# Optimization experiments

Measured on AMD Instinct MI355X. Metric: run time of the kernel, lower is better.

## Reference

```python
import jax, jax.numpy as jnp
import numpy as np
from math import ceil, sqrt

# Inner module: Linear(2048,4096)+ReLU, Linear(4096,4096)+ReLU, Linear(4096,2048)
D_IN, D_H, D_OUT = 2048, 4096, 2048
BATCH = 4096
# named_modules() order: each Linear yields weight then bias; ReLU skipped
SHAPES = [(D_H, D_IN), (D_H,), (D_H, D_H), (D_H,), (D_OUT, D_H), (D_OUT,)]
NUM_P = sum(int(np.prod(s)) for s in SHAPES)  # 33_566_720
SIZE_N = ceil(sqrt(NUM_P))                    # 5794
SIZE_M = ceil(1.0 * SIZE_N / 2)               # 2897 (compress = 1.0)


def setup_inputs() -> dict:
    key = jax.random.key(0)
    k1, k2, k3 = jax.random.split(key, 3)
    k = sqrt(12) / 2 * SIZE_M ** (-0.25)  # norm_V init bound
    V1 = jax.random.uniform(k1, (SIZE_N, SIZE_M), jnp.float32, -k, k)
    V2 = jax.random.uniform(k2, (SIZE_M, SIZE_N), jnp.float32, -k, k)
    x = jax.random.normal(k3, (BATCH, D_IN), jnp.float32)
    return {"x": x, "V1": V1, "V2": V2}


def _unpack(Vf):
    # scatter-copy: contiguous slices of flattened V -> weights/biases in traversal order
    params, i = [], 0
    for s in SHAPES:
        n = int(np.prod(s))
        params.append(Vf[i:i + n].reshape(s))
        i += n
    return params


def reference(x, V1, V2):
    # WandBtoV: low-rank reconstruction then per-element copy into weights (fused here)
    Vf = (V1 @ V2).reshape(-1)  # [SIZE_N*SIZE_N]; only first NUM_P elements used
    W1, b1, W2, b2, W3, b3 = _unpack(Vf)
    h = jax.nn.relu(x @ W1.T + b1)   # [B, D_H]
    h = jax.nn.relu(h @ W2.T + b2)   # [B, D_H]
    return h @ W3.T + b3             # [B, D_OUT]
```

## Files before the change

### kernel.cpp

```cpp
#include <hip/hip_runtime.h>
#include <stdint.h>

typedef __attribute__((ext_vector_type(8)))  __bf16 bf16x8;
typedef __attribute__((ext_vector_type(16))) float  f32x16;
typedef unsigned short u16;
typedef __attribute__((ext_vector_type(8))) unsigned short u16x8;

#define GLOBAL_AS __attribute__((address_space(1)))
#define LDS_AS    __attribute__((address_space(3)))

__device__ __forceinline__ void load_lds16(const void* g, void* l) {
    __builtin_amdgcn_global_load_lds((const GLOBAL_AS void*)g, (LDS_AS void*)l, 16, 0, 0);
}

__device__ __forceinline__ u16 f2bf(float f) {
    union { float f; uint32_t u; } v; v.f = f;
    uint32_t r = v.u + 0x7FFFu + ((v.u >> 16) & 1u);
    return (u16)(r >> 16);
}
__device__ __forceinline__ float b2f(u16 b) {
    union { uint32_t u; float f; } v; v.u = ((uint32_t)b) << 16;
    return v.f;
}

__global__ void k_conv_pad(const float* __restrict__ in, u16* __restrict__ out,
                           int rIn, int cIn, int cOut, int total8) {
    int idx = blockIdx.x * blockDim.x + threadIdx.x;
    if (idx >= total8) return;
    int c8n = cOut >> 3;
    int r  = idx / c8n;
    int c0 = (idx - r * c8n) << 3;
    u16x8 o;
#pragma unroll
    for (int j = 0; j < 8; ++j) {
        int c = c0 + j;
        o[j] = (r < rIn && c < cIn) ? f2bf(in[(size_t)r * cIn + c]) : (u16)0;
    }
    *(u16x8*)(out + (size_t)r * cOut + c0) = o;
}

__global__ void k_transpose_conv(const float* __restrict__ in, u16* __restrict__ out,
                                 int kIn, int nIn, int kOut) {
    __shared__ float tile[32][33];
    int k0 = blockIdx.x * 32, n0 = blockIdx.y * 32;
    int tx = threadIdx.x, ty = threadIdx.y;
#pragma unroll
    for (int i = 0; i < 4; ++i) {
        int k = k0 + ty + i * 8, n = n0 + tx;
        tile[ty + i * 8][tx] = (k < kIn && n < nIn) ? in[(size_t)k * nIn + n] : 0.f;
    }
    __syncthreads();
#pragma unroll
    for (int i = 0; i < 4; ++i) {
        int n = n0 + ty + i * 8, k = k0 + tx;
        out[(size_t)n * kOut + k] = f2bf(tile[tx][ty + i * 8]);
    }
}

template <int MODE>
__global__ __launch_bounds__(256, 4) void k_gemm_bt(
    const u16* __restrict__ A, const u16* __restrict__ B,
    const u16* __restrict__ bias, void* __restrict__ Cv,
    int K, int ldc, int mReal, int nReal) {
    (void)bias;
    __shared__ __align__(16) char lds[32768];
    char* As = lds;
    char* Bs = lds + 16384;

    const int tid  = threadIdx.x;
    const int w    = tid >> 6, lane = tid & 63;
    const int l31  = lane & 31, hi = lane >> 5;
    const int wm   = (w & 1) * 64, wn = (w >> 1) * 64;
    const int bm   = blockIdx.y * 128, bn = blockIdx.x * 128;

    const int srcRow = tid >> 3;
    const int srcCol = (tid & 7) ^ (srcRow & 7);
    const u16* aSrc = A + (size_t)(bm + srcRow) * K + (srcCol << 3);
    const u16* bSrc = B + (size_t)(bn + srcRow) * K + (srcCol << 3);
    char* aDst = As + ((tid & ~63) << 4);
    char* bDst = Bs + ((tid & ~63) << 4);

    const int aRow0 = (wm + l31) * 128;
    const int aRow1 = (wm + 32 + l31) * 128;
    const int bRow0 = (wn + l31) * 128;
    const int bRow1 = (wn + 32 + l31) * 128;

    f32x16 acc[2][2];
#pragma unroll
    for (int i = 0; i < 2; ++i)
#pragma unroll
        for (int j = 0; j < 2; ++j) acc[i][j] = (f32x16)(0.f);

    for (int k0 = 0; k0 < K; k0 += 64) {
#pragma unroll
        for (int t = 0; t < 4; ++t) {
            load_lds16(aSrc + (size_t)(t * 32) * K, aDst + t * 4096);
            load_lds16(bSrc + (size_t)(t * 32) * K, bDst + t * 4096);
        }
        aSrc += 64; bSrc += 64;
        __syncthreads();
#pragma unroll
        for (int ks = 0; ks < 4; ++ks) {
            const int swz = (((ks * 2 + hi) ^ (l31 & 7)) << 4);
            bf16x8 af[2], bfr[2];
            af[0]  = *(const bf16x8*)(As + aRow0 + swz);
            af[1]  = *(const bf16x8*)(As + aRow1 + swz);
            bfr[0] = *(const bf16x8*)(Bs + bRow0 + swz);
            bfr[1] = *(const bf16x8*)(Bs + bRow1 + swz);
#pragma unroll
            for (int mi = 0; mi < 2; ++mi)
#pragma unroll
                for (int ni = 0; ni < 2; ++ni)
                    acc[mi][ni] = __builtin_amdgcn_mfma_f32_32x32x16_bf16(
                        af[mi], bfr[ni], acc[mi][ni], 0, 0, 0);
        }
        __syncthreads();
    }

    float bv[2];
    if (MODE >= 1) {
#pragma unroll
        for (int ni = 0; ni < 2; ++ni) bv[ni] = b2f(bias[bn + wn + ni * 32 + l31]);
    }
#pragma unroll
    for (int mi = 0; mi < 2; ++mi) {
#pragma unroll
        for (int reg = 0; reg < 16; ++reg) {
            int row = bm + wm + mi * 32 + (reg & 3) + 8 * (reg >> 2) + 4 * hi;
#pragma unroll
            for (int ni = 0; ni < 2; ++ni) {
                int col = bn + wn + ni * 32 + l31;
                float v = acc[mi][ni][reg];
                if (MODE == 0) {
                    if (row < mReal && col < nReal)
                        ((u16*)Cv)[(size_t)row * ldc + col] = f2bf(v);
                } else if (MODE == 1) {
                    v += bv[ni];
                    v = v > 0.f ? v : 0.f;
                    ((u16*)Cv)[(size_t)row * ldc + col] = f2bf(v);
                } else {
                    ((float*)Cv)[(size_t)row * ldc + col] = v + bv[ni];
                }
            }
        }
    }
}

extern "C" void kernel_launch(void* const* d_in, const int* in_sizes, int n_in,
                              void* d_out, int out_size, void* d_ws, size_t ws_size,
                              hipStream_t stream) {
    (void)in_sizes; (void)n_in; (void)out_size; (void)ws_size;
    const float* x  = (const float*)d_in[0];
    const float* V1 = (const float*)d_in[1];
    const float* V2 = (const float*)d_in[2];

    char* ws = (char*)d_ws;
    u16* Vf   = (u16*)(ws);
    u16* V1b  = (u16*)(ws + 67141120);
    u16* V2bT = (u16*)(ws + 67141120 + 34668544);
    u16* Xb   = (u16*)(ws + 67141120 + 2 * 34668544);
    u16* H1   = V1b;
    u16* H2   = V2bT;

    k_conv_pad<<<8464, 256, 0, stream>>>(V1, V1b, 5794, 2897, 2944, 5888 * 2944 / 8);
    k_transpose_conv<<<dim3(92, 184), dim3(32, 8), 0, stream>>>(V2, V2bT, 2897, 5794, 2944);
    k_conv_pad<<<4096, 256, 0, stream>>>(x, Xb, 4096, 2048, 2048, 4096 * 2048 / 8);

    k_gemm_bt<0><<<dim3(46, 46), 256, 0, stream>>>(V1b, V2bT, nullptr, Vf,
                                                   2944, 5794, 5794, 5794);
    k_gemm_bt<1><<<dim3(32, 32), 256, 0, stream>>>(Xb, Vf + 0, Vf + 8388608, H1,
                                                   2048, 4096, 4096, 4096);
    k_gemm_bt<1><<<dim3(32, 32), 256, 0, stream>>>(H1, Vf + 8392704, Vf + 25169920, H2,
                                                   4096, 4096, 4096, 4096);
    k_gemm_bt<2><<<dim3(16, 32), 256, 0, stream>>>(H2, Vf + 25174016, Vf + 33562624, d_out,
                                                   4096, 2048, 4096, 2048);
}
```

Measured before the change: 795.3 us.

## Add 256x256 double-buffered 8-wave GEMM with XCD-aware tile remap

Adds a new GEMM kernel that uses 256x256 output tiles with 8 waves per block and double-buffered 128KB LDS. Global-to-LDS loads for the next stage overlap with MFMA work, fenced by explicit vmcnt/lgkmcnt waits and barriers, and s_setprio raises priority around the MFMA bursts. Block IDs are remapped so that consecutive tiles land on the same XCD. The first three GEMMs use the new kernel, while the last layer keeps the old 128x128 kernel. In exchange, occupancy is lower, register use is higher, and the 5794-size GEMM pads to 23x23 tiles, which adds wasted work at the edges.

```diff
diff --git a/kernel.cpp b/kernel.cpp
--- a/kernel.cpp
+++ b/kernel.cpp
@@ -146,6 +146,142 @@
     }
 }
 
+
+#define BARRIER() do { asm volatile("" ::: "memory"); \
+                       __builtin_amdgcn_s_barrier(); \
+                       asm volatile("" ::: "memory"); } while (0)
+#define LGKM0()   do { asm volatile("s_waitcnt lgkmcnt(0)" ::: "memory"); \
+                       __builtin_amdgcn_sched_barrier(0); } while (0)
+#define VMCNT(n)  asm volatile("s_waitcnt vmcnt(" #n ")" ::: "memory")
+
+#define STAGE8(bb, ko) do { \
+    _Pragma("unroll") for (int t = 0; t < 4; ++t) \
+        load_lds16(aS + (ko) + (size_t)(t * 64) * K, (bb) + wOff + t * 8192); \
+    _Pragma("unroll") for (int t = 0; t < 4; ++t) \
+        load_lds16(bS + (ko) + (size_t)(t * 64) * K, (bb) + 32768 + wOff + t * 8192); \
+} while (0)
+
+#define PH_RD_A(bb, mh) do { \
+    _Pragma("unroll") for (int m2 = 0; m2 < 2; ++m2) \
+    _Pragma("unroll") for (int ks = 0; ks < 4; ++ks) \
+        fa[m2][ks] = *(const bf16x8*)((bb) + aRowB + ((mh) * 2 + m2) * 4096 + (chB ^ (ks << 5))); \
+} while (0)
+
+#define PH_RD_B(bb, n) do { \
+    _Pragma("unroll") for (int ks = 0; ks < 4; ++ks) \
+        fb[n][ks] = *(const bf16x8*)((bb) + bRowB + (n) * 4096 + (chB ^ (ks << 5))); \
+} while (0)
+
+#define PH_MM(mh, n) do { \
+    __builtin_amdgcn_s_setprio(1); \
+    _Pragma("unroll") for (int m2 = 0; m2 < 2; ++m2) \
+    _Pragma("unroll") for (int ks = 0; ks < 4; ++ks) \
+        acc[(mh) * 2 + m2][n] = __builtin_amdgcn_mfma_f32_32x32x16_bf16( \
+            fa[m2][ks], fb[n][ks], acc[(mh) * 2 + m2][n], 0, 0, 0); \
+    __builtin_amdgcn_s_setprio(0); \
+} while (0)
+
+template <int MODE>
+__global__ __launch_bounds__(512, 2) void k_gemm256(
+    const u16* __restrict__ A, const u16* __restrict__ B,
+    const u16* __restrict__ bias, void* __restrict__ Cv,
+    int K, int ldc, int mReal, int nReal, int gx) {
+    __shared__ __align__(16) char lds[131072];
+
+    const int tid  = threadIdx.x;
+    const int w    = tid >> 6, lane = tid & 63;
+    const int l31  = lane & 31, hi = lane >> 5;
+    const int wr   = w & 1, wc = w >> 1;
+
+    const int nwg = (int)gridDim.x;
+    const int q   = nwg >> 3, r = nwg & 7;
+    const int xcd = (int)blockIdx.x & 7, lid = (int)blockIdx.x >> 3;
+    const int wg  = (xcd < r ? xcd * (q + 1) : r * (q + 1) + (xcd - r) * q) + lid;
+    const int bm  = (wg / gx) * 256;
+    const int bn  = (wg % gx) * 256;
+
+    char* const buf0 = lds;
+    char* const buf1 = lds + 65536;
+
+    const int srcRow = tid >> 3;
+    const int srcCh  = (tid & 7) ^ (srcRow & 7);
+    const u16* const aS = A + (size_t)(bm + srcRow) * K + (srcCh << 3);
+    const u16* const bS = B + (size_t)(bn + srcRow) * K + (srcCh << 3);
+    const int wOff = (tid & ~63) << 4;
+
+    const int aRowB = (wr * 128 + l31) * 128;
+    const int bRowB = 32768 + (wc * 64 + l31) * 128;
+    const int chB   = (hi ^ (l31 & 7)) << 4;
+
+    f32x16 acc[4][2];
+#pragma unroll
+    for (int i = 0; i < 4; ++i)
+#pragma unroll
+        for (int j = 0; j < 2; ++j) acc[i][j] = (f32x16)(0.f);
+
+    bf16x8 fa[2][4], fb[2][4];
+
+    STAGE8(buf0, 0);
+    STAGE8(buf1, 64);
+    VMCNT(8);
+    BARRIER();
+
+    const int nIt = K >> 7;
+    size_t ko = 128;
+#pragma unroll 1
+    for (int it = 0; it < nIt; ++it) {
+        const bool notLast = (it != nIt - 1);
+        PH_RD_A(buf0, 0); PH_RD_B(buf0, 0);
+        BARRIER(); LGKM0(); PH_MM(0, 0); BARRIER();
+        PH_RD_B(buf0, 1);
+        BARRIER(); LGKM0(); PH_MM(0, 1); BARRIER();
+        PH_RD_A(buf0, 1);
+        BARRIER(); LGKM0(); PH_MM(1, 1); BARRIER();
+        if (notLast) { STAGE8(buf0, ko); }
+        BARRIER(); PH_MM(1, 0);
+        if (notLast) { VMCNT(8); } else { VMCNT(0); }
+        BARRIER();
+        PH_RD_A(buf1, 0); PH_RD_B(buf1, 0);
+        BARRIER(); LGKM0(); PH_MM(0, 0); BARRIER();
+        PH_RD_B(buf1, 1);
+        BARRIER(); LGKM0(); PH_MM(0, 1); BARRIER();
+        PH_RD_A(buf1, 1);
+        BARRIER(); LGKM0(); PH_MM(1, 1); BARRIER();
+        if (notLast) { STAGE8(buf1, ko + 64); ko += 128; }
+        BARRIER(); PH_MM(1, 0);
+        if (notLast) { VMCNT(8); }
+        BARRIER();
+    }
+
+    float bv[2];
+    if (MODE >= 1) {
+#pragma unroll
+        for (int ni = 0; ni < 2; ++ni) bv[ni] = b2f(bias[bn + wc * 64 + ni * 32 + l31]);
+    }
+#pragma unroll
+    for (int mi = 0; mi < 4; ++mi) {
+#pragma unroll
+        for (int reg = 0; reg < 16; ++reg) {
+            const int row = bm + wr * 128 + mi * 32 + (reg & 3) + 8 * (reg >> 2) + 4 * hi;
+#pragma unroll
+            for (int ni = 0; ni < 2; ++ni) {
+                const int col = bn + wc * 64 + ni * 32 + l31;
+                float v = acc[mi][ni][reg];
+                if (MODE == 0) {
+                    if (row < mReal && col < nReal)
+                        ((u16*)Cv)[(size_t)row * ldc + col] = f2bf(v);
+                } else if (MODE == 1) {
+                    v += bv[ni];
+                    v = v > 0.f ? v : 0.f;
+                    ((u16*)Cv)[(size_t)row * ldc + col] = f2bf(v);
+                } else {
+                    ((float*)Cv)[(size_t)row * ldc + col] = v + bv[ni];
+                }
+            }
+        }
+    }
+}
+
 extern "C" void kernel_launch(void* const* d_in, const int* in_sizes, int n_in,
                               void* d_out, int out_size, void* d_ws, size_t ws_size,
                               hipStream_t stream) {
@@ -166,12 +302,12 @@
     k_transpose_conv<<<dim3(92, 184), dim3(32, 8), 0, stream>>>(V2, V2bT, 2897, 5794, 2944);
     k_conv_pad<<<4096, 256, 0, stream>>>(x, Xb, 4096, 2048, 2048, 4096 * 2048 / 8);
 
-    k_gemm_bt<0><<<dim3(46, 46), 256, 0, stream>>>(V1b, V2bT, nullptr, Vf,
-                                                   2944, 5794, 5794, 5794);
-    k_gemm_bt<1><<<dim3(32, 32), 256, 0, stream>>>(Xb, Vf + 0, Vf + 8388608, H1,
-                                                   2048, 4096, 4096, 4096);
-    k_gemm_bt<1><<<dim3(32, 32), 256, 0, stream>>>(H1, Vf + 8392704, Vf + 25169920, H2,
-                                                   4096, 4096, 4096, 4096);
+    k_gemm256<0><<<529, 512, 0, stream>>>(V1b, V2bT, nullptr, Vf,
+                                          2944, 5794, 5794, 5794, 23);
+    k_gemm256<1><<<256, 512, 0, stream>>>(Xb, Vf + 0, Vf + 8388608, H1,
+                                          2048, 4096, 4096, 4096, 16);
+    k_gemm256<1><<<256, 512, 0, stream>>>(H1, Vf + 8392704, Vf + 25169920, H2,
+                                          4096, 4096, 4096, 4096, 16);
     k_gemm_bt<2><<<dim3(16, 32), 256, 0, stream>>>(H2, Vf + 25174016, Vf + 33562624, d_out,
                                                    4096, 2048, 4096, 2048);
 }
```

Result: no change. 790.5 us (-0.6%).

## Replace first three GEMMs with double-buffered 256x256 ping-pong MFMA kernel

Applied to the files above, without the earlier changes.

Adds a new 512-thread GEMM kernel with 256x256 output tiles and two 64-deep K stages in 128KB of LDS. It interleaves global-to-LDS loads with 16x16x32 bf16 MFMA blocks, using explicit waitcnt, barriers and setprio. Blocks are remapped across XCDs and loop persistently over tiles. This targets the low reuse and exposed load latency of the old single-buffered 128x128 kernel in the V1@V2 reconstruction and the first two MLP layers. In exchange it uses much more LDS and registers, allowing only one block per CU, and the hand-tuned synchronization is fragile.

```diff
diff --git a/kernel.cpp b/kernel.cpp
--- a/kernel.cpp
+++ b/kernel.cpp
@@ -2,6 +2,7 @@
 #include <stdint.h>
 
 typedef __attribute__((ext_vector_type(8)))  __bf16 bf16x8;
+typedef __attribute__((ext_vector_type(4)))  float  f32x4;
 typedef __attribute__((ext_vector_type(16))) float  f32x16;
 typedef unsigned short u16;
 typedef __attribute__((ext_vector_type(8))) unsigned short u16x8;
@@ -146,6 +147,146 @@
     }
 }
 
+
+#define BARRIER() do { asm volatile("" ::: "memory"); \
+                       __builtin_amdgcn_s_barrier(); \
+                       asm volatile("" ::: "memory"); } while (0)
+#define LGKM0()   do { asm volatile("s_waitcnt lgkmcnt(0)" ::: "memory"); \
+                       __builtin_amdgcn_sched_barrier(0); } while (0)
+#define LGKM8()   do { asm volatile("s_waitcnt lgkmcnt(8)" ::: "memory"); \
+                       __builtin_amdgcn_sched_barrier(0); } while (0)
+#define VMCNT(n)  do { asm volatile("s_waitcnt vmcnt(" #n ")" ::: "memory"); \
+                       __builtin_amdgcn_sched_barrier(0); } while (0)
+
+#define STG_A(BUFB, H, KT) do { \
+    load_lds16(aStage + (size_t)((H) * 128)      * K + (KT), lds + (BUFB) * 65536 + (H) * 16384 +        ldsW); \
+    load_lds16(aStage + (size_t)((H) * 128 + 64) * K + (KT), lds + (BUFB) * 65536 + (H) * 16384 + 8192 + ldsW); \
+} while (0)
+#define STG_B(BUFB, H, KT) do { \
+    load_lds16(bStage + (size_t)((H) * 128)      * K + (KT), lds + (BUFB) * 65536 + 32768 + (H) * 16384 +        ldsW); \
+    load_lds16(bStage + (size_t)((H) * 128 + 64) * K + (KT), lds + (BUFB) * 65536 + 32768 + (H) * 16384 + 8192 + ldsW); \
+} while (0)
+
+#define RDA(BUFB, MH) do { \
+    _Pragma("unroll") for (int m2 = 0; m2 < 4; ++m2) { \
+        a[m2][0] = *(const bf16x8*)(lds + (BUFB) * 65536 + aWave + (MH) * 8192 + m2 * 2048 + laneF); \
+        a[m2][1] = *(const bf16x8*)(lds + (BUFB) * 65536 + aWave + (MH) * 8192 + m2 * 2048 + (laneF ^ 64)); \
+    } } while (0)
+#define RDB(BUFB, NH, DST) do { \
+    _Pragma("unroll") for (int n2 = 0; n2 < 2; ++n2) { \
+        DST[n2][0] = *(const bf16x8*)(lds + (BUFB) * 65536 + bWave + (NH) * 4096 + n2 * 2048 + laneF); \
+        DST[n2][1] = *(const bf16x8*)(lds + (BUFB) * 65536 + bWave + (NH) * 4096 + n2 * 2048 + (laneF ^ 64)); \
+    } } while (0)
+
+#define MM16(AA, BB, MH, NH) do { \
+    __builtin_amdgcn_s_setprio(1); \
+    _Pragma("unroll") for (int ks = 0; ks < 2; ++ks) \
+    _Pragma("unroll") for (int n2 = 0; n2 < 2; ++n2) \
+    _Pragma("unroll") for (int m2 = 0; m2 < 4; ++m2) \
+        acc[(MH) * 4 + m2][(NH) * 2 + n2] = __builtin_amdgcn_mfma_f32_16x16x32_bf16( \
+            AA[m2][ks], BB[n2][ks], acc[(MH) * 4 + m2][(NH) * 2 + n2], 0, 0, 0); \
+    __builtin_amdgcn_s_setprio(0); \
+} while (0)
+
+template <int MODE>
+__global__ __launch_bounds__(512, 2) void k_gemm8p(
+    const u16* __restrict__ A, const u16* __restrict__ B,
+    const u16* __restrict__ bias, void* __restrict__ Cv,
+    int K, int ldc, int mReal, int nReal, int gx, int nTiles) {
+    __shared__ __align__(16) char lds[131072];
+
+    const int tid  = threadIdx.x;
+    const int w    = tid >> 6, lane = tid & 63;
+    const int wc   = w & 3, wr = w >> 2;
+    const int l15  = lane & 15, lg4 = lane >> 4;
+
+    const int nwg = (int)gridDim.x;
+    const int q   = nwg >> 3, r = nwg & 7;
+    const int xcd = (int)blockIdx.x & 7, lid = (int)blockIdx.x >> 3;
+    const int wg0 = (xcd < r ? xcd * (q + 1) : r * (q + 1) + (xcd - r) * q) + lid;
+
+    const int laneF = l15 * 128 + (((lane >> 4) ^ (lane & 7)) << 4);
+    const int aWave = wr * 16384;
+    const int bWave = 32768 + (wc >> 1) * 16384 + (wc & 1) * 8192;
+
+    const int cOrig = (lane & 7) ^ ((lane >> 3) & 7);
+    const int sRow  = w * 8 + (lane >> 3);
+    const int ldsW  = w * 1024;
+
+    const int nIt = K >> 7;
+
+    for (int v = wg0; v < nTiles; v += (int)gridDim.x) {
+        const int bm = (v / gx) * 256;
+        const int bn = (v % gx) * 256;
+        const u16* const aStage = A + (size_t)(bm + sRow) * K + cOrig * 8;
+        const u16* const bStage = B + (size_t)(bn + sRow) * K + cOrig * 8;
+
+        f32x4 acc[8][4];
+#pragma unroll
+        for (int i = 0; i < 8; ++i)
+#pragma unroll
+            for (int j = 0; j < 4; ++j) acc[i][j] = (f32x4)(0.f);
+
+        bf16x8 a[4][2], b0[2][2], b1[2][2];
+
+        STG_A(0, 0, 0);  STG_B(0, 0, 0);  STG_A(0, 1, 0);  STG_B(0, 1, 0);
+        STG_B(1, 0, 64); STG_B(1, 1, 64);
+        VMCNT(4);
+        BARRIER();
+
+#pragma unroll 1
+        for (int it = 0; it < nIt; ++it) {
+            const bool ok = (it + 1 < nIt);
+            const size_t kT1 = (size_t)(2 * it + 1) * 64;
+            const size_t kS  = (size_t)(2 * it + 2) * 64;
+            RDA(0, 0); RDB(0, 0, b0); STG_A(1, 0, kT1);
+            LGKM8(); BARRIER(); LGKM0(); MM16(a, b0, 0, 0); BARRIER();
+            RDB(0, 1, b1); STG_A(1, 1, kT1);
+            BARRIER(); LGKM0(); MM16(a, b1, 0, 1); BARRIER();
+            RDA(0, 1); if (ok) { STG_B(0, 0, kS); }
+            BARRIER(); LGKM0(); MM16(a, b1, 1, 1); BARRIER();
+            if (ok) { STG_B(0, 1, kS); VMCNT(4); } else { VMCNT(0); }
+            BARRIER(); MM16(a, b0, 1, 0); BARRIER();
+            RDA(1, 0); RDB(1, 0, b0); if (ok) { STG_A(0, 0, kS); }
+            LGKM8(); BARRIER(); LGKM0(); MM16(a, b0, 0, 0); BARRIER();
+            RDB(1, 1, b1); if (ok) { STG_A(0, 1, kS); }
+            BARRIER(); LGKM0(); MM16(a, b1, 0, 1); BARRIER();
+            RDA(1, 1); if (ok) { STG_B(1, 0, kS + 64); }
+            BARRIER(); LGKM0(); MM16(a, b1, 1, 1); BARRIER();
+            if (ok) { STG_B(1, 1, kS + 64); VMCNT(4); }
+            BARRIER(); MM16(a, b0, 1, 0); BARRIER();
+        }
+
+        float bv[4];
+        if (MODE >= 1) {
+#pragma unroll
+            for (int ni = 0; ni < 4; ++ni) bv[ni] = b2f(bias[bn + wc * 64 + ni * 16 + l15]);
+        }
+#pragma unroll
+        for (int mi = 0; mi < 8; ++mi) {
+#pragma unroll
+            for (int ni = 0; ni < 4; ++ni) {
+#pragma unroll
+                for (int rg = 0; rg < 4; ++rg) {
+                    const int row = bm + wr * 128 + mi * 16 + lg4 * 4 + rg;
+                    const int col = bn + wc * 64 + ni * 16 + l15;
+                    float vv = acc[mi][ni][rg];
+                    if (MODE == 0) {
+                        if (row < mReal && col < nReal)
+                            ((u16*)Cv)[(size_t)row * ldc + col] = f2bf(vv);
+                    } else if (MODE == 1) {
+                        vv += bv[ni];
+                        vv = vv > 0.f ? vv : 0.f;
+                        ((u16*)Cv)[(size_t)row * ldc + col] = f2bf(vv);
+                    } else {
+                        ((float*)Cv)[(size_t)row * ldc + col] = vv + bv[ni];
+                    }
+                }
+            }
+        }
+    }
+}
+
 extern "C" void kernel_launch(void* const* d_in, const int* in_sizes, int n_in,
                               void* d_out, int out_size, void* d_ws, size_t ws_size,
                               hipStream_t stream) {
@@ -166,12 +307,12 @@
     k_transpose_conv<<<dim3(92, 184), dim3(32, 8), 0, stream>>>(V2, V2bT, 2897, 5794, 2944);
     k_conv_pad<<<4096, 256, 0, stream>>>(x, Xb, 4096, 2048, 2048, 4096 * 2048 / 8);
 
-    k_gemm_bt<0><<<dim3(46, 46), 256, 0, stream>>>(V1b, V2bT, nullptr, Vf,
-                                                   2944, 5794, 5794, 5794);
-    k_gemm_bt<1><<<dim3(32, 32), 256, 0, stream>>>(Xb, Vf + 0, Vf + 8388608, H1,
-                                                   2048, 4096, 4096, 4096);
-    k_gemm_bt<1><<<dim3(32, 32), 256, 0, stream>>>(H1, Vf + 8392704, Vf + 25169920, H2,
-                                                   4096, 4096, 4096, 4096);
+    k_gemm8p<0><<<512, 512, 0, stream>>>(V1b, V2bT, nullptr, Vf,
+                                         2944, 5794, 5794, 5794, 23, 529);
+    k_gemm8p<1><<<256, 512, 0, stream>>>(Xb, Vf + 0, Vf + 8388608, H1,
+                                         2048, 4096, 4096, 4096, 16, 256);
+    k_gemm8p<1><<<256, 512, 0, stream>>>(H1, Vf + 8392704, Vf + 25169920, H2,
+                                         4096, 4096, 4096, 4096, 16, 256);
     k_gemm_bt<2><<<dim3(16, 32), 256, 0, stream>>>(H2, Vf + 25174016, Vf + 33562624, d_out,
                                                    4096, 2048, 4096, 2048);
 }
```

After: 700.5 us. -11.9%, faster.
